# Performance work log

Measured on AMD Instinct MI355X. Metric: run time of the kernel, lower is better.

Reference implementation:

```python
import jax, jax.numpy as jnp
import numpy as np

B, L, H, N = 4, 4096, 1024, 16
EPS = 1e-6  # layer_norm_epsilon


def setup_inputs() -> dict:
    key = jax.random.key(0)
    ks = jax.random.split(key, 8)
    hidden_states = jax.random.normal(ks[0], (B, L, H), dtype=jnp.float32)
    attention_mask = jnp.ones((B, L), dtype=jnp.float32)
    norm_weight = jnp.ones((H,), dtype=jnp.float32)
    # S4D init: dt log-uniform in [1e-3, 1e-1]; S4D-Lin A init; random C, D
    dt_min, dt_max = 1e-3, 1e-1
    log_dt = jax.random.uniform(ks[1], (H,), dtype=jnp.float32) * (
        float(np.log(dt_max)) - float(np.log(dt_min))) + float(np.log(dt_min))
    log_A_real = jnp.log(0.5 * jnp.ones((H, N), dtype=jnp.float32))
    A_imag = jnp.broadcast_to(float(np.pi) * jnp.arange(N, dtype=jnp.float32), (H, N))
    C_real = jax.random.normal(ks[2], (H, N), dtype=jnp.float32) * (0.5 ** 0.5)
    C_imag = jax.random.normal(ks[3], (H, N), dtype=jnp.float32) * (0.5 ** 0.5)
    D = jax.random.normal(ks[4], (H,), dtype=jnp.float32)
    out_w = jax.random.normal(ks[5], (2 * H, H), dtype=jnp.float32) * 0.02  # 1x1 conv to 2H (GLU)
    out_b = jnp.zeros((2 * H,), dtype=jnp.float32)
    return dict(hidden_states=hidden_states, attention_mask=attention_mask,
                norm_weight=norm_weight, log_dt=log_dt, log_A_real=log_A_real,
                A_imag=A_imag, C_real=C_real, C_imag=C_imag, D=D,
                out_w=out_w, out_b=out_b)


def _s4d_kernel(log_dt, log_A_real, A_imag, C_real, C_imag, length):
    """Diagonal SSM convolution kernel k[h, l] (S4D ZOH discretization)."""
    dt = jnp.exp(log_dt)                                   # (H,)
    A = -jnp.exp(log_A_real) + 1j * A_imag                 # (H, N) complex64
    C = C_real + 1j * C_imag                               # (H, N)
    dtA = A * dt[:, None]                                  # (H, N)
    C_disc = C * (jnp.exp(dtA) - 1.0) / A                  # (H, N)
    vand = jnp.exp(dtA[:, :, None] * jnp.arange(length, dtype=jnp.float32))  # (H, N, L)
    k = 2.0 * jnp.einsum('hn,hnl->hl', C_disc, vand).real  # (H, L)
    return k.astype(jnp.float32)


def reference(hidden_states, attention_mask, norm_weight, log_dt, log_A_real,
              A_imag, C_real, C_imag, D, out_w, out_b):
    # LongT5LayerNorm: RMSNorm (no mean subtraction), variance in fp32
    var = jnp.mean(jnp.square(hidden_states.astype(jnp.float32)), axis=-1, keepdims=True)
    normed = hidden_states * jax.lax.rsqrt(var + EPS) * norm_weight  # (B, L, H)
    # mask padded positions, go to channel-major layout (B, H, L)
    u = (normed * attention_mask[..., None]).transpose(0, 2, 1)
    Lx = u.shape[-1]
    k = _s4d_kernel(log_dt, log_A_real, A_imag, C_real, C_imag, Lx)  # (H, L)
    # causal convolution via FFT of length 2L
    nfft = 2 * Lx
    k_f = jnp.fft.rfft(k, n=nfft)                 # (H, nfft//2+1)
    u_f = jnp.fft.rfft(u, n=nfft)                 # (B, H, nfft//2+1)
    y = jnp.fft.irfft(u_f * k_f, n=nfft)[..., :Lx]  # (B, H, L)
    y = y + u * D[:, None]                        # skip connection
    y = jax.nn.gelu(y, approximate=False)         # torch nn.GELU (exact)
    # output 1x1 conv to 2H, then GLU over the channel dim
    z = jnp.einsum('bhl,oh->bol', y, out_w) + out_b[:, None]
    a, b = jnp.split(z, 2, axis=1)
    ssm_out = (a * jax.nn.sigmoid(b)).transpose(0, 2, 1)  # (B, L, H)
    # residual + dropout (eval mode -> identity)
    return hidden_states + ssm_out
```

## Files before the change

kernel.cpp:

```cpp
#include <hip/hip_runtime.h>

#define B_   4
#define L_   4096
#define H_   1024
#define N_   16
#define CH_  128
#define NC_  (L_/CH_)
#define M_   (B_*L_)
#define O2_  (2*H_)
#define EPS_ 1e-6f

typedef __attribute__((ext_vector_type(4))) float  f32x4;
typedef __attribute__((ext_vector_type(8))) __bf16 bf16x8;

__device__ __forceinline__ unsigned short f2bf(float x) {
  union { float f; unsigned int u; } v; v.f = x;
  unsigned int r = v.u + 0x7FFFu + ((v.u >> 16) & 1u);
  return (unsigned short)(r >> 16);
}

__device__ __forceinline__ void async_copy16(const void* g, void* l) {
  __builtin_amdgcn_global_load_lds(
      (const __attribute__((address_space(1))) unsigned int*)g,
      (__attribute__((address_space(3))) unsigned int*)l, 16, 0, 0);
}

__global__ void k_params(const float* __restrict__ log_dt,
                         const float* __restrict__ log_A_real,
                         const float* __restrict__ A_imag,
                         const float* __restrict__ C_real,
                         const float* __restrict__ C_imag,
                         float* __restrict__ wr,  float* __restrict__ wi,
                         float* __restrict__ c2r, float* __restrict__ c2i,
                         float* __restrict__ wpr, float* __restrict__ wpi) {
  int idx = blockIdx.x * 256 + threadIdx.x;
  if (idx >= H_ * N_) return;
  int h = idx / N_, n = idx % N_;
  int hn = h * N_ + n;
  float dt  = expf(log_dt[h]);
  float Ar  = -expf(log_A_real[hn]);
  float Ai  = A_imag[hn];
  float dr  = Ar * dt, di = Ai * dt;
  float er  = expf(dr);
  float wrv = er * cosf(di), wiv = er * sinf(di);
  float e1r = wrv - 1.0f, e1i = wiv;
  float den = Ar * Ar + Ai * Ai;
  float qr  = (e1r * Ar + e1i * Ai) / den;
  float qi  = (e1i * Ar - e1r * Ai) / den;
  float Cr  = C_real[hn], Ci = C_imag[hn];
  float cdr = Cr * qr - Ci * qi;
  float cdi = Cr * qi + Ci * qr;
  float ep  = expf((float)CH_ * dr);
  int o = n * H_ + h;
  wr[o]  = wrv;  wi[o]  = wiv;
  c2r[o] = 2.0f * cdr; c2i[o] = 2.0f * cdi;
  wpr[o] = ep * cosf((float)CH_ * di);
  wpi[o] = ep * sinf((float)CH_ * di);
}

__global__ void k_wbf(const float* __restrict__ w, unsigned short* __restrict__ wb) {
  int i = blockIdx.x * 256 + threadIdx.x;
  wb[i] = f2bf(w[i]);
}

__global__ __launch_bounds__(256) void k_scale(const float* __restrict__ hs,
                                               const float* __restrict__ mask,
                                               float* __restrict__ scale) {
  int m = blockIdx.x, tid = threadIdx.x;
  float4 v = reinterpret_cast<const float4*>(hs + (size_t)m * H_)[tid];
  float s = v.x * v.x + v.y * v.y + v.z * v.z + v.w * v.w;
  #pragma unroll
  for (int off = 32; off > 0; off >>= 1) s += __shfl_down(s, off, 64);
  __shared__ float ps[4];
  if ((tid & 63) == 0) ps[tid >> 6] = s;
  __syncthreads();
  if (tid == 0) {
    float var = (ps[0] + ps[1] + ps[2] + ps[3]) * (1.0f / H_);
    scale[m] = rsqrtf(var + EPS_) * mask[m];
  }
}

__global__ __launch_bounds__(256) void k_scan1(const float* __restrict__ hs,
                                               const float* __restrict__ nw,
                                               const float* __restrict__ scale,
                                               const float* __restrict__ wr_,
                                               const float* __restrict__ wi_,
                                               float* __restrict__ endr,
                                               float* __restrict__ endi) {
  int tid = threadIdx.x;
  int h = blockIdx.x * 256 + tid;
  int c = blockIdx.y, b = blockIdx.z;
  float wr[N_], wi[N_], xr[N_], xi[N_];
  #pragma unroll
  for (int n = 0; n < N_; n++) {
    wr[n] = wr_[n * H_ + h]; wi[n] = wi_[n * H_ + h];
    xr[n] = 0.f; xi[n] = 0.f;
  }
  float nwh = nw[h];
  __shared__ float ssc[CH_];
  int l0 = c * CH_;
  if (tid < CH_) ssc[tid] = scale[(size_t)b * L_ + l0 + tid];
  __syncthreads();
  const float* hp = hs + ((size_t)b * L_ + l0) * H_ + h;
  #pragma unroll 8
  for (int l = 0; l < CH_; l++) {
    float u = hp[(size_t)l * H_] * ssc[l] * nwh;
    #pragma unroll
    for (int n = 0; n < N_; n++) {
      float oxr = xr[n];
      xr[n] = fmaf(wr[n], oxr, fmaf(-wi[n], xi[n], u));
      xi[n] = fmaf(wr[n], xi[n], wi[n] * oxr);
    }
  }
  size_t base = (((size_t)b * NC_ + c) * N_) * H_ + h;
  #pragma unroll
  for (int n = 0; n < N_; n++) {
    endr[base + (size_t)n * H_] = xr[n];
    endi[base + (size_t)n * H_] = xi[n];
  }
}

__global__ __launch_bounds__(256) void k_carry(const float* __restrict__ wpr_,
                                               const float* __restrict__ wpi_,
                                               const float* __restrict__ endr,
                                               const float* __restrict__ endi,
                                               float* __restrict__ carr,
                                               float* __restrict__ cari) {
  int idx = blockIdx.x * 256 + threadIdx.x;
  int b = idx >> 10, h = idx & (H_ - 1);
  float wpr[N_], wpi[N_], sr[N_], si[N_];
  #pragma unroll
  for (int n = 0; n < N_; n++) {
    wpr[n] = wpr_[n * H_ + h]; wpi[n] = wpi_[n * H_ + h];
    sr[n] = 0.f; si[n] = 0.f;
  }
  for (int c = 0; c < NC_; c++) {
    size_t base = (((size_t)b * NC_ + c) * N_) * H_ + h;
    #pragma unroll
    for (int n = 0; n < N_; n++) {
      carr[base + (size_t)n * H_] = sr[n];
      cari[base + (size_t)n * H_] = si[n];
      float er = endr[base + (size_t)n * H_];
      float ei = endi[base + (size_t)n * H_];
      float osr = sr[n];
      sr[n] = fmaf(wpr[n], osr,  fmaf(-wpi[n], si[n], er));
      si[n] = fmaf(wpr[n], si[n], fmaf(wpi[n], osr, ei));
    }
  }
}

__global__ __launch_bounds__(256) void k_scan2(const float* __restrict__ hs,
                                               const float* __restrict__ nw,
                                               const float* __restrict__ scale,
                                               const float* __restrict__ wr_,
                                               const float* __restrict__ wi_,
                                               const float* __restrict__ c2r_,
                                               const float* __restrict__ c2i_,
                                               const float* __restrict__ Dp,
                                               const float* __restrict__ carr,
                                               const float* __restrict__ cari,
                                               unsigned short* __restrict__ ybf) {
  int tid = threadIdx.x;
  int h = blockIdx.x * 256 + tid;
  int c = blockIdx.y, b = blockIdx.z;
  float wr[N_], wi[N_], cr[N_], ci[N_], xr[N_], xi[N_];
  size_t base = (((size_t)b * NC_ + c) * N_) * H_ + h;
  #pragma unroll
  for (int n = 0; n < N_; n++) {
    wr[n] = wr_[n * H_ + h]; wi[n] = wi_[n * H_ + h];
    cr[n] = c2r_[n * H_ + h]; ci[n] = c2i_[n * H_ + h];
    xr[n] = carr[base + (size_t)n * H_];
    xi[n] = cari[base + (size_t)n * H_];
  }
  float nwh = nw[h], Dh = Dp[h];
  __shared__ float ssc[CH_];
  int l0 = c * CH_;
  if (tid < CH_) ssc[tid] = scale[(size_t)b * L_ + l0 + tid];
  __syncthreads();
  const float* hp = hs + ((size_t)b * L_ + l0) * H_ + h;
  unsigned short* yp = ybf + ((size_t)b * L_ + l0) * H_ + h;
  #pragma unroll 4
  for (int l = 0; l < CH_; l++) {
    float u = hp[(size_t)l * H_] * ssc[l] * nwh;
    float yv = u * Dh;
    #pragma unroll
    for (int n = 0; n < N_; n++) {
      float oxr = xr[n];
      xr[n] = fmaf(wr[n], oxr, fmaf(-wi[n], xi[n], u));
      xi[n] = fmaf(wr[n], xi[n], wi[n] * oxr);
      yv = fmaf(cr[n], xr[n], yv);
      yv = fmaf(-ci[n], xi[n], yv);
    }
    float g = 0.5f * yv * (1.0f + erff(yv * 0.70710678118654752f));
    yp[(size_t)l * H_] = f2bf(g);
  }
}

#define BM 128
#define BN 128
#define BK 32
__global__ __launch_bounds__(256) void k_gemm(const unsigned short* __restrict__ A,
                                              const unsigned short* __restrict__ Bw,
                                              float* __restrict__ Z) {
  __shared__ __align__(16) unsigned short As[BM * BK];
  __shared__ __align__(16) unsigned short Bs[BN * BK];
  const int tid  = threadIdx.x;
  const int lane = tid & 63;
  const int wave = tid >> 6;
  const int bn = blockIdx.x * BN;
  const int bm = blockIdx.y * BM;
  const int wm = (wave >> 1) * 64;
  const int wn = (wave & 1) * 64;
  const int K = H_;
  f32x4 acc[4][4];
  #pragma unroll
  for (int mi = 0; mi < 4; mi++)
    #pragma unroll
    for (int ni = 0; ni < 4; ni++) acc[mi][ni] = (f32x4){0.f, 0.f, 0.f, 0.f};

  const int g0 = tid, g1 = 256 + tid;
  const int r0 = g0 >> 2, q0 = (g0 & 3) * 8;
  const int r1 = g1 >> 2, q1 = (g1 & 3) * 8;
  const int ar = lane & 15, kq = (lane >> 4) * 8;

  for (int k0 = 0; k0 < K; k0 += BK) {
    async_copy16(A  + (size_t)(bm + r0) * K + k0 + q0, &As[g0 * 8]);
    async_copy16(A  + (size_t)(bm + r1) * K + k0 + q1, &As[g1 * 8]);
    async_copy16(Bw + (size_t)(bn + r0) * K + k0 + q0, &Bs[g0 * 8]);
    async_copy16(Bw + (size_t)(bn + r1) * K + k0 + q1, &Bs[g1 * 8]);
    __syncthreads();
    bf16x8 af[4], bf[4];
    #pragma unroll
    for (int mi = 0; mi < 4; mi++)
      af[mi] = *reinterpret_cast<const bf16x8*>(&As[(wm + mi * 16 + ar) * BK + kq]);
    #pragma unroll
    for (int ni = 0; ni < 4; ni++)
      bf[ni] = *reinterpret_cast<const bf16x8*>(&Bs[(wn + ni * 16 + ar) * BK + kq]);
    #pragma unroll
    for (int mi = 0; mi < 4; mi++)
      #pragma unroll
      for (int ni = 0; ni < 4; ni++)
        acc[mi][ni] = __builtin_amdgcn_mfma_f32_16x16x32_bf16(af[mi], bf[ni], acc[mi][ni], 0, 0, 0);
    __syncthreads();
  }
  #pragma unroll
  for (int mi = 0; mi < 4; mi++)
    #pragma unroll
    for (int ni = 0; ni < 4; ni++)
      #pragma unroll
      for (int r = 0; r < 4; r++) {
        int m = bm + wm + mi * 16 + (lane >> 4) * 4 + r;
        int o = bn + wn + ni * 16 + (lane & 15);
        Z[(size_t)m * O2_ + o] = acc[mi][ni][r];
      }
}

__global__ __launch_bounds__(256) void k_glu(const float* __restrict__ Z,
                                             const float* __restrict__ ob,
                                             const float* __restrict__ hs,
                                             float* __restrict__ out) {
  size_t i4 = (size_t)blockIdx.x * 256 + threadIdx.x;
  size_t m = i4 >> 8;
  int hq = (int)(i4 & 255);
  const float4* zr = reinterpret_cast<const float4*>(Z + m * O2_);
  float4 a  = zr[hq];
  float4 bb = zr[256 + hq];
  const float4* ob4 = reinterpret_cast<const float4*>(ob);
  float4 oa = ob4[hq], obv = ob4[256 + hq];
  float4 hv = reinterpret_cast<const float4*>(hs)[i4];
  float4 r;
  r.x = hv.x + (a.x + oa.x) / (1.0f + __expf(-(bb.x + obv.x)));
  r.y = hv.y + (a.y + oa.y) / (1.0f + __expf(-(bb.y + obv.y)));
  r.z = hv.z + (a.z + oa.z) / (1.0f + __expf(-(bb.z + obv.z)));
  r.w = hv.w + (a.w + oa.w) / (1.0f + __expf(-(bb.w + obv.w)));
  reinterpret_cast<float4*>(out)[i4] = r;
}

extern "C" void kernel_launch(void* const* d_in, const int* in_sizes, int n_in,
                              void* d_out, int out_size, void* d_ws, size_t ws_size,
                              hipStream_t stream) {
  const float* hs    = (const float*)d_in[0];
  const float* mask  = (const float*)d_in[1];
  const float* nw    = (const float*)d_in[2];
  const float* ldt   = (const float*)d_in[3];
  const float* lar   = (const float*)d_in[4];
  const float* aim   = (const float*)d_in[5];
  const float* crl   = (const float*)d_in[6];
  const float* cim   = (const float*)d_in[7];
  const float* Dp    = (const float*)d_in[8];
  const float* outw  = (const float*)d_in[9];
  const float* outb  = (const float*)d_in[10];
  float* out = (float*)d_out;

  size_t off = 0;
  char* ws = (char*)d_ws;
  auto nxt = [&](size_t bytes) -> void* {
    void* p = ws + off; off += (bytes + 255) & ~(size_t)255; return p;
  };
  float* wr   = (float*)nxt(H_ * N_ * 4);
  float* wi   = (float*)nxt(H_ * N_ * 4);
  float* c2r  = (float*)nxt(H_ * N_ * 4);
  float* c2i  = (float*)nxt(H_ * N_ * 4);
  float* wpr  = (float*)nxt(H_ * N_ * 4);
  float* wpi  = (float*)nxt(H_ * N_ * 4);
  float* scale= (float*)nxt((size_t)M_ * 4);
  float* endr = (float*)nxt((size_t)B_ * NC_ * N_ * H_ * 4);
  float* endi = (float*)nxt((size_t)B_ * NC_ * N_ * H_ * 4);
  float* carr = (float*)nxt((size_t)B_ * NC_ * N_ * H_ * 4);
  float* cari = (float*)nxt((size_t)B_ * NC_ * N_ * H_ * 4);
  unsigned short* Wbf = (unsigned short*)nxt((size_t)O2_ * H_ * 2);
  unsigned short* ybf = (unsigned short*)nxt((size_t)M_ * H_ * 2);
  float* Z    = (float*)nxt((size_t)M_ * O2_ * 4);

  k_params<<<dim3(H_ * N_ / 256), dim3(256), 0, stream>>>(ldt, lar, aim, crl, cim,
                                                          wr, wi, c2r, c2i, wpr, wpi);
  k_wbf<<<dim3(O2_ * H_ / 256), dim3(256), 0, stream>>>(outw, Wbf);
  k_scale<<<dim3(M_), dim3(256), 0, stream>>>(hs, mask, scale);
  k_scan1<<<dim3(H_ / 256, NC_, B_), dim3(256), 0, stream>>>(hs, nw, scale, wr, wi, endr, endi);
  k_carry<<<dim3(B_ * H_ / 256), dim3(256), 0, stream>>>(wpr, wpi, endr, endi, carr, cari);
  k_scan2<<<dim3(H_ / 256, NC_, B_), dim3(256), 0, stream>>>(hs, nw, scale, wr, wi, c2r, c2i,
                                                             Dp, carr, cari, ybf);
  k_gemm<<<dim3(O2_ / BN, M_ / BM), dim3(256), 0, stream>>>(ybf, Wbf, Z);
  k_glu<<<dim3((size_t)M_ * H_ / 4 / 256), dim3(256), 0, stream>>>(Z, outb, hs, out);
}
```

Before: 421.2 us.

## Fuse GLU epilogue into GEMM, interleave weights, swizzle LDS, parallelize carry

The output weight rows are interleaved so each GLU gate/value pair sits in adjacent GEMM columns. The GLU, bias and residual are then computed in the GEMM epilogue through a lane shuffle, which removes the 128 MB Z intermediate and the separate k_glu pass. The parameter and weight conversion kernels are merged into one launch. k_carry now runs one thread per (b,n,h) instead of per (b,h) for more parallelism, and the LDS tiles use an XOR swizzle to reduce bank conflicts. The cost is that half the lanes sit idle during the epilogue and the output stores are strided rather than vectorized.

```diff
diff --git a/kernel.cpp b/kernel.cpp
--- a/kernel.cpp
+++ b/kernel.cpp
@@ -25,42 +25,46 @@
       (__attribute__((address_space(3))) unsigned int*)l, 16, 0, 0);
 }
 
-__global__ void k_params(const float* __restrict__ log_dt,
-                         const float* __restrict__ log_A_real,
-                         const float* __restrict__ A_imag,
-                         const float* __restrict__ C_real,
-                         const float* __restrict__ C_imag,
-                         float* __restrict__ wr,  float* __restrict__ wi,
-                         float* __restrict__ c2r, float* __restrict__ c2i,
-                         float* __restrict__ wpr, float* __restrict__ wpi) {
+__global__ void k_prep(const float* __restrict__ log_dt,
+                       const float* __restrict__ log_A_real,
+                       const float* __restrict__ A_imag,
+                       const float* __restrict__ C_real,
+                       const float* __restrict__ C_imag,
+                       const float* __restrict__ outw,
+                       const float* __restrict__ outb,
+                       float* __restrict__ wr,  float* __restrict__ wi,
+                       float* __restrict__ c2r, float* __restrict__ c2i,
+                       float* __restrict__ wpr, float* __restrict__ wpi,
+                       unsigned short* __restrict__ Wbf,
+                       float* __restrict__ bp) {
   int idx = blockIdx.x * 256 + threadIdx.x;
-  if (idx >= H_ * N_) return;
-  int h = idx / N_, n = idx % N_;
-  int hn = h * N_ + n;
-  float dt  = expf(log_dt[h]);
-  float Ar  = -expf(log_A_real[hn]);
-  float Ai  = A_imag[hn];
-  float dr  = Ar * dt, di = Ai * dt;
-  float er  = expf(dr);
-  float wrv = er * cosf(di), wiv = er * sinf(di);
-  float e1r = wrv - 1.0f, e1i = wiv;
-  float den = Ar * Ar + Ai * Ai;
-  float qr  = (e1r * Ar + e1i * Ai) / den;
-  float qi  = (e1i * Ar - e1r * Ai) / den;
-  float Cr  = C_real[hn], Ci = C_imag[hn];
-  float cdr = Cr * qr - Ci * qi;
-  float cdi = Cr * qi + Ci * qr;
-  float ep  = expf((float)CH_ * dr);
-  int o = n * H_ + h;
-  wr[o]  = wrv;  wi[o]  = wiv;
-  c2r[o] = 2.0f * cdr; c2i[o] = 2.0f * cdi;
-  wpr[o] = ep * cosf((float)CH_ * di);
-  wpi[o] = ep * sinf((float)CH_ * di);
-}
-
-__global__ void k_wbf(const float* __restrict__ w, unsigned short* __restrict__ wb) {
-  int i = blockIdx.x * 256 + threadIdx.x;
-  wb[i] = f2bf(w[i]);
+  int p = idx >> 10, hh = idx & (H_ - 1);
+  size_t src = (size_t)((p >> 1) + (p & 1) * H_) * H_ + hh;
+  Wbf[idx] = f2bf(outw[src]);
+  if (idx < O2_) bp[idx] = outb[(idx >> 1) + (idx & 1) * H_];
+  if (idx < H_ * N_) {
+    int h = idx / N_, n = idx % N_;
+    int hn = h * N_ + n;
+    float dt  = expf(log_dt[h]);
+    float Ar  = -expf(log_A_real[hn]);
+    float Ai  = A_imag[hn];
+    float dr  = Ar * dt, di = Ai * dt;
+    float er  = expf(dr);
+    float wrv = er * cosf(di), wiv = er * sinf(di);
+    float e1r = wrv - 1.0f, e1i = wiv;
+    float den = Ar * Ar + Ai * Ai;
+    float qr  = (e1r * Ar + e1i * Ai) / den;
+    float qi  = (e1i * Ar - e1r * Ai) / den;
+    float Cr  = C_real[hn], Ci = C_imag[hn];
+    float cdr = Cr * qr - Ci * qi;
+    float cdi = Cr * qi + Ci * qr;
+    float ep  = expf((float)CH_ * dr);
+    int o = n * H_ + h;
+    wr[o]  = wrv;  wi[o]  = wiv;
+    c2r[o] = 2.0f * cdr; c2i[o] = 2.0f * cdi;
+    wpr[o] = ep * cosf((float)CH_ * di);
+    wpi[o] = ep * sinf((float)CH_ * di);
+  }
 }
 
 __global__ __launch_bounds__(256) void k_scale(const float* __restrict__ hs,
@@ -127,25 +131,19 @@
                                                float* __restrict__ carr,
                                                float* __restrict__ cari) {
   int idx = blockIdx.x * 256 + threadIdx.x;
-  int b = idx >> 10, h = idx & (H_ - 1);
-  float wpr[N_], wpi[N_], sr[N_], si[N_];
-  #pragma unroll
-  for (int n = 0; n < N_; n++) {
-    wpr[n] = wpr_[n * H_ + h]; wpi[n] = wpi_[n * H_ + h];
-    sr[n] = 0.f; si[n] = 0.f;
-  }
-  for (int c = 0; c < NC_; c++) {
-    size_t base = (((size_t)b * NC_ + c) * N_) * H_ + h;
-    #pragma unroll
-    for (int n = 0; n < N_; n++) {
-      carr[base + (size_t)n * H_] = sr[n];
-      cari[base + (size_t)n * H_] = si[n];
-      float er = endr[base + (size_t)n * H_];
-      float ei = endi[base + (size_t)n * H_];
-      float osr = sr[n];
-      sr[n] = fmaf(wpr[n], osr,  fmaf(-wpi[n], si[n], er));
-      si[n] = fmaf(wpr[n], si[n], fmaf(wpi[n], osr, ei));
-    }
+  int h = idx & (H_ - 1);
+  int n = (idx >> 10) & (N_ - 1);
+  int b = idx >> 14;
+  float wprv = wpr_[n * H_ + h], wpiv = wpi_[n * H_ + h];
+  float sr = 0.f, si = 0.f;
+  size_t cstride = (size_t)N_ * H_;
+  size_t base = ((size_t)b * NC_) * cstride + (size_t)n * H_ + h;
+  for (int c = 0; c < NC_; c++, base += cstride) {
+    carr[base] = sr; cari[base] = si;
+    float er = endr[base], ei = endi[base];
+    float osr = sr;
+    sr = fmaf(wprv, osr,  fmaf(-wpiv, si, er));
+    si = fmaf(wprv, si, fmaf(wpiv, osr, ei));
   }
 }
 
@@ -201,7 +199,9 @@
 #define BK 32
 __global__ __launch_bounds__(256) void k_gemm(const unsigned short* __restrict__ A,
                                               const unsigned short* __restrict__ Bw,
-                                              float* __restrict__ Z) {
+                                              const float* __restrict__ bp,
+                                              const float* __restrict__ hs,
+                                              float* __restrict__ out) {
   __shared__ __align__(16) unsigned short As[BM * BK];
   __shared__ __align__(16) unsigned short Bs[BN * BK];
   const int tid  = threadIdx.x;
@@ -219,23 +219,27 @@
     for (int ni = 0; ni < 4; ni++) acc[mi][ni] = (f32x4){0.f, 0.f, 0.f, 0.f};
 
   const int g0 = tid, g1 = 256 + tid;
-  const int r0 = g0 >> 2, q0 = (g0 & 3) * 8;
-  const int r1 = g1 >> 2, q1 = (g1 & 3) * 8;
-  const int ar = lane & 15, kq = (lane >> 4) * 8;
+  const int r0 = g0 >> 2, c0 = ((g0 & 3) ^ ((r0 >> 1) & 3)) * 8;
+  const int r1 = g1 >> 2, c1 = ((g1 & 3) ^ ((r1 >> 1) & 3)) * 8;
+  const int ar = lane & 15, kqi = lane >> 4;
 
   for (int k0 = 0; k0 < K; k0 += BK) {
-    async_copy16(A  + (size_t)(bm + r0) * K + k0 + q0, &As[g0 * 8]);
-    async_copy16(A  + (size_t)(bm + r1) * K + k0 + q1, &As[g1 * 8]);
-    async_copy16(Bw + (size_t)(bn + r0) * K + k0 + q0, &Bs[g0 * 8]);
-    async_copy16(Bw + (size_t)(bn + r1) * K + k0 + q1, &Bs[g1 * 8]);
+    async_copy16(A  + (size_t)(bm + r0) * K + k0 + c0, &As[g0 * 8]);
+    async_copy16(A  + (size_t)(bm + r1) * K + k0 + c1, &As[g1 * 8]);
+    async_copy16(Bw + (size_t)(bn + r0) * K + k0 + c0, &Bs[g0 * 8]);
+    async_copy16(Bw + (size_t)(bn + r1) * K + k0 + c1, &Bs[g1 * 8]);
     __syncthreads();
     bf16x8 af[4], bf[4];
     #pragma unroll
-    for (int mi = 0; mi < 4; mi++)
-      af[mi] = *reinterpret_cast<const bf16x8*>(&As[(wm + mi * 16 + ar) * BK + kq]);
-    #pragma unroll
-    for (int ni = 0; ni < 4; ni++)
-      bf[ni] = *reinterpret_cast<const bf16x8*>(&Bs[(wn + ni * 16 + ar) * BK + kq]);
+    for (int mi = 0; mi < 4; mi++) {
+      int row = wm + mi * 16 + ar;
+      af[mi] = *reinterpret_cast<const bf16x8*>(&As[row * BK + ((kqi ^ ((row >> 1) & 3)) * 8)]);
+    }
+    #pragma unroll
+    for (int ni = 0; ni < 4; ni++) {
+      int row = wn + ni * 16 + ar;
+      bf[ni] = *reinterpret_cast<const bf16x8*>(&Bs[row * BK + ((kqi ^ ((row >> 1) & 3)) * 8)]);
+    }
     #pragma unroll
     for (int mi = 0; mi < 4; mi++)
       #pragma unroll
@@ -244,36 +248,26 @@
     __syncthreads();
   }
   #pragma unroll
-  for (int mi = 0; mi < 4; mi++)
-    #pragma unroll
-    for (int ni = 0; ni < 4; ni++)
+  for (int mi = 0; mi < 4; mi++) {
+    int mrow0 = bm + wm + mi * 16 + (lane >> 4) * 4;
+    #pragma unroll
+    for (int ni = 0; ni < 4; ni++) {
+      int p  = bn + wn + ni * 16 + (lane & 15);
+      int pe = p & ~1;
+      float bA = bp[pe], bB = bp[pe + 1];
+      int j = pe >> 1;
       #pragma unroll
       for (int r = 0; r < 4; r++) {
-        int m = bm + wm + mi * 16 + (lane >> 4) * 4 + r;
-        int o = bn + wn + ni * 16 + (lane & 15);
-        Z[(size_t)m * O2_ + o] = acc[mi][ni][r];
+        float v = acc[mi][ni][r];
+        float w = __shfl_xor(v, 1, 64);
+        if (!(lane & 1)) {
+          float g = (v + bA) / (1.0f + __expf(-(w + bB)));
+          size_t o = (size_t)(mrow0 + r) * H_ + j;
+          out[o] = hs[o] + g;
+        }
       }
-}
-
-__global__ __launch_bounds__(256) void k_glu(const float* __restrict__ Z,
-                                             const float* __restrict__ ob,
-                                             const float* __restrict__ hs,
-                                             float* __restrict__ out) {
-  size_t i4 = (size_t)blockIdx.x * 256 + threadIdx.x;
-  size_t m = i4 >> 8;
-  int hq = (int)(i4 & 255);
-  const float4* zr = reinterpret_cast<const float4*>(Z + m * O2_);
-  float4 a  = zr[hq];
-  float4 bb = zr[256 + hq];
-  const float4* ob4 = reinterpret_cast<const float4*>(ob);
-  float4 oa = ob4[hq], obv = ob4[256 + hq];
-  float4 hv = reinterpret_cast<const float4*>(hs)[i4];
-  float4 r;
-  r.x = hv.x + (a.x + oa.x) / (1.0f + __expf(-(bb.x + obv.x)));
-  r.y = hv.y + (a.y + oa.y) / (1.0f + __expf(-(bb.y + obv.y)));
-  r.z = hv.z + (a.z + oa.z) / (1.0f + __expf(-(bb.z + obv.z)));
-  r.w = hv.w + (a.w + oa.w) / (1.0f + __expf(-(bb.w + obv.w)));
-  reinterpret_cast<float4*>(out)[i4] = r;
+    }
+  }
 }
 
 extern "C" void kernel_launch(void* const* d_in, const int* in_sizes, int n_in,
@@ -303,6 +297,7 @@
   float* c2i  = (float*)nxt(H_ * N_ * 4);
   float* wpr  = (float*)nxt(H_ * N_ * 4);
   float* wpi  = (float*)nxt(H_ * N_ * 4);
+  float* bpck = (float*)nxt(O2_ * 4);
   float* scale= (float*)nxt((size_t)M_ * 4);
   float* endr = (float*)nxt((size_t)B_ * NC_ * N_ * H_ * 4);
   float* endi = (float*)nxt((size_t)B_ * NC_ * N_ * H_ * 4);
@@ -310,16 +305,15 @@
   float* cari = (float*)nxt((size_t)B_ * NC_ * N_ * H_ * 4);
   unsigned short* Wbf = (unsigned short*)nxt((size_t)O2_ * H_ * 2);
   unsigned short* ybf = (unsigned short*)nxt((size_t)M_ * H_ * 2);
-  float* Z    = (float*)nxt((size_t)M_ * O2_ * 4);
-
-  k_params<<<dim3(H_ * N_ / 256), dim3(256), 0, stream>>>(ldt, lar, aim, crl, cim,
-                                                          wr, wi, c2r, c2i, wpr, wpi);
-  k_wbf<<<dim3(O2_ * H_ / 256), dim3(256), 0, stream>>>(outw, Wbf);
+
+  k_prep<<<dim3(O2_ * H_ / 256), dim3(256), 0, stream>>>(ldt, lar, aim, crl, cim,
+                                                         outw, outb,
+                                                         wr, wi, c2r, c2i, wpr, wpi,
+                                                         Wbf, bpck);
   k_scale<<<dim3(M_), dim3(256), 0, stream>>>(hs, mask, scale);
   k_scan1<<<dim3(H_ / 256, NC_, B_), dim3(256), 0, stream>>>(hs, nw, scale, wr, wi, endr, endi);
-  k_carry<<<dim3(B_ * H_ / 256), dim3(256), 0, stream>>>(wpr, wpi, endr, endi, carr, cari);
+  k_carry<<<dim3(B_ * N_ * H_ / 256), dim3(256), 0, stream>>>(wpr, wpi, endr, endi, carr, cari);
   k_scan2<<<dim3(H_ / 256, NC_, B_), dim3(256), 0, stream>>>(hs, nw, scale, wr, wi, c2r, c2i,
                                                              Dp, carr, cari, ybf);
-  k_gemm<<<dim3(O2_ / BN, M_ / BM), dim3(256), 0, stream>>>(ybf, Wbf, Z);
-  k_glu<<<dim3((size_t)M_ * H_ / 4 / 256), dim3(256), 0, stream>>>(Z, outb, hs, out);
-}
+  k_gemm<<<dim3(O2_ / BN, M_ / BM), dim3(256), 0, stream>>>(ybf, Wbf, bpck, hs, out);
+}
```

Measured after the change: 386.5 us. 8.2% less time.
